# Kernel optimization log

Hardware: AMD Instinct MI355X
Metric: run time of the kernel (lower is better)

The kernel has to match this reference:

```python
import jax, jax.numpy as jnp
import numpy as np

GMAX, EMAX, NATOM, AA = 4, 10, 14, 20
SCALE_CLAMP = 0.1
EPS = 1e-8


def setup_inputs() -> dict:
    key = jax.random.key(0)
    ks = jax.random.split(key, 10)
    B, N, H = 4, 16384, 256
    rng = np.random.default_rng(0)
    # per-AA kinematic metadata (mimics pack_residue_meta_for_batch output)
    G_counts = rng.integers(1, GMAX + 1, size=AA).astype(np.int32)
    tors_axis = np.full((AA, GMAX, 2), -1, np.int32)
    aff_idx = np.zeros((AA, GMAX, EMAX), np.int32)
    aff_mask = np.zeros((AA, GMAX, EMAX), bool)
    for a in range(AA):
        for g in range(int(G_counts[a])):
            tors_axis[a, g] = rng.permutation(NATOM)[:2]
            perm = rng.permutation(NATOM)[:EMAX]  # unique affected atoms
            ne = int(rng.integers(3, EMAX + 1))
            aff_idx[a, g, :ne] = perm[:ne]
            aff_mask[a, g, :ne] = True
    scale_mask = rng.random((AA, NATOM)) < 0.5
    scale_parent = rng.integers(0, NATOM, size=(AA, NATOM)).astype(np.int32)

    s = 0.05
    ap = jax.random.uniform(ks[1], (B, N, AA), jnp.float32)
    return {
        'h': jax.random.normal(ks[0], (B, N, H), jnp.float32),
        'aatype_probs': ap / ap.sum(-1, keepdims=True),
        'X': jax.random.normal(ks[2], (B, N, NATOM, 3), jnp.float32),
        'W1': jax.random.normal(ks[3], (H + AA, H), jnp.float32) * s,
        'b1': jnp.zeros((H,), jnp.float32),
        'W2': jax.random.normal(ks[4], (H, H), jnp.float32) * s,
        'b2': jnp.zeros((H,), jnp.float32),
        'Wt': jax.random.normal(ks[5], (H, GMAX), jnp.float32) * s,
        'bt': jnp.zeros((GMAX,), jnp.float32),
        'Ws': jax.random.normal(ks[6], (H, NATOM), jnp.float32) * s,
        'bs': jnp.zeros((NATOM,), jnp.float32),
        'exists': jax.random.uniform(ks[7], (B, N, NATOM)) < 0.9,
        'top_idx': jax.random.randint(ks[8], (B, N), 0, AA, jnp.int32),
        'tors_axis': jnp.asarray(tors_axis),
        'aff_idx': jnp.asarray(aff_idx),
        'aff_mask': jnp.asarray(aff_mask),
        'G_counts': jnp.asarray(G_counts),
        'scale_mask': jnp.asarray(scale_mask),
        'scale_parent': jnp.asarray(scale_parent),
    }


def _take(X, idx):
    # X: [B,N,14,3], idx: [B,N,K] -> [B,N,K,3]
    return jnp.take_along_axis(X, jnp.broadcast_to(idx[..., None], idx.shape + (3,)), axis=2)


def _fk(X, exists, dchi, sraw, top_idx, TA, AI, AM, GC, SM, SP):
    B, N = top_idx.shape
    bi = jnp.arange(B)[:, None, None]
    ni = jnp.arange(N)[None, :, None]
    g_mask = jnp.arange(GMAX) < GC[..., None]  # [B,N,Gmax]
    for gi in range(GMAX):
        u, v = TA[..., gi, 0], TA[..., gi, 1]
        axis_ok = (u >= 0) & (v >= 0) & g_mask[..., gi]
        Pu = _take(X, jnp.maximum(u, 0)[..., None])  # [B,N,1,3]
        Pv = _take(X, jnp.maximum(v, 0)[..., None])
        axis = Pv - Pu
        axisn = axis / jnp.maximum(jnp.linalg.norm(axis, axis=-1, keepdims=True), EPS)
        ang = jnp.where(axis_ok, dchi[..., gi], 0.0)[..., None, None]  # [B,N,1,1]
        cols = jnp.maximum(AI[..., gi, :], 0)  # [B,N,E]
        cmask = AM[..., gi, :]
        Xa = _take(X, cols)          # [B,N,E,3]
        Va = Xa - Pu
        cos, sin = jnp.cos(ang), jnp.sin(ang)
        cross = jnp.cross(jnp.broadcast_to(axisn, Va.shape), Va, axis=-1)
        dot = jnp.sum(Va * axisn, -1, keepdims=True)
        Xa_new = Pu + Va * cos + cross * sin + axisn * dot * (1.0 - cos)
        ex_cols = jnp.take_along_axis(exists, cols, axis=2)
        wmask = cmask & ex_cols
        safe_cols = jnp.where(wmask, cols, NATOM)  # OOB -> dropped
        X = X.at[bi, ni, safe_cols].set(Xa_new, mode='drop')
    # bond-length scaling toward parent atom
    SPc = jnp.maximum(SP, 0)
    Pp = _take(X, SPc)               # [B,N,14,3]
    vvec = X - Pp
    r = jnp.maximum(jnp.linalg.norm(vvec, axis=-1, keepdims=True), EPS)
    dirv = vvec / r
    s_eff = jnp.clip(sraw, -1.0, 1.0) * SCALE_CLAMP
    Pa_new = Pp + dirv * r * (1.0 + s_eff[..., None])
    pair_exist = exists & jnp.take_along_axis(exists, SPc, axis=2)
    W = (SM & pair_exist)[..., None]
    return jnp.where(W, Pa_new, X)


def reference(h, aatype_probs, X, W1, b1, W2, b2, Wt, bt, Ws, bs,
              exists, top_idx, tors_axis, aff_idx, aff_mask, G_counts,
              scale_mask, scale_parent):
    # TorsionScaleHead
    z = jnp.concatenate([h, aatype_probs], axis=-1)
    z = jax.nn.silu(z @ W1 + b1)
    z = jax.nn.silu(z @ W2 + b2)
    dchi = jnp.tanh(z @ Wt + bt) * 0.5      # [B,N,Gmax]
    sraw = jnp.tanh(z @ Ws + bs)            # [B,N,14]
    # gather per-residue metadata
    TA = tors_axis[top_idx]
    AI = aff_idx[top_idx]
    AM = aff_mask[top_idx]
    GC = G_counts[top_idx]
    SM = scale_mask[top_idx]
    SP = scale_parent[top_idx]
    return _fk(X, exists, dchi, sraw, top_idx, TA, AI, AM, GC, SM, SP)
```

## Files before the change

kernel.cpp:

```cpp
#include <hip/hip_runtime.h>
#include <hip/hip_bf16.h>
#include <stdint.h>

#define TM 64
#define NT 512
#define HDIM 256
#define HA 276
#define HAP 288
#define ZROW 296
#define AAC 20
#define GMAXC 4
#define EMAXC 10
#define NATOMC 14

#define W1T_OFF 0
#define W2T_OFF 73728
#define W3T_OFF 139264
#define WS_ELEMS 147456

#define ZH_OFF  0
#define ZL_OFF  37888
#define XS_OFF  37888
#define EXS_OFF 48640
#define TSS_OFF 75776
#define SMEM_BYTES 80640

typedef __attribute__((ext_vector_type(8))) short bf16x8;
typedef __attribute__((ext_vector_type(4))) short short4v;
typedef __attribute__((ext_vector_type(4))) float f32x4;

__device__ __forceinline__ float silu_f(float x) {
    return x * (1.0f / (1.0f + __expf(-x)));
}

__device__ __forceinline__ float tanh_fast(float x) {
    float e = __expf(2.0f * x);
    return 1.0f - 2.0f / (e + 1.0f);
}

__device__ __forceinline__ unsigned short f2bf(float f) {
    union { float f; unsigned int u; } x; x.f = f;
    unsigned int r = x.u + 0x7fffu + ((x.u >> 16) & 1u);
    return (unsigned short)(r >> 16);
}

__device__ __forceinline__ float bf2f(unsigned short s) {
    union { unsigned int u; float f; } x; x.u = ((unsigned int)s) << 16;
    return x.f;
}

template <bool SPLIT>
__global__ __launch_bounds__(256) void prep_weights(
    const float* __restrict__ W1, const float* __restrict__ W2,
    const float* __restrict__ Wt, const float* __restrict__ Ws,
    unsigned short* __restrict__ ws)
{
    int idx = blockIdx.x * 256 + threadIdx.x;
    if (idx >= WS_ELEMS) return;
    float v;
    if (idx < W2T_OFF) {
        int n = idx / HAP, k = idx - n * HAP;
        v = (k < HA) ? W1[(size_t)k * HDIM + n] : 0.0f;
    } else if (idx < W3T_OFF) {
        int i = idx - W2T_OFF;
        int n = i / HDIM, k = i - n * HDIM;
        v = W2[(size_t)k * HDIM + n];
    } else {
        int i = idx - W3T_OFF;
        int n = i / HDIM, k = i - n * HDIM;
        v = (n < GMAXC) ? Wt[(size_t)k * GMAXC + n]
          : (n < GMAXC + NATOMC) ? Ws[(size_t)k * NATOMC + (n - GMAXC)]
          : 0.0f;
    }
    unsigned short hi = f2bf(v);
    ws[idx] = hi;
    if (SPLIT) ws[WS_ELEMS + idx] = f2bf(v - bf2f(hi));
}

template <bool SPLIT>
__global__ __launch_bounds__(NT, 4) void fused_refiner(
    const float* __restrict__ h,
    const float* __restrict__ probs,
    const float* __restrict__ X,
    const unsigned short* __restrict__ ws,
    const float* __restrict__ b1,
    const float* __restrict__ b2,
    const float* __restrict__ bt,
    const float* __restrict__ bs,
    const int* __restrict__ exists,
    const int* __restrict__ top_idx,
    const int* __restrict__ TA,
    const int* __restrict__ AI,
    const int* __restrict__ AM,
    const int* __restrict__ GC,
    const int* __restrict__ SM,
    const int* __restrict__ SP,
    float* __restrict__ out)
{
    __shared__ __align__(16) unsigned char smem[SMEM_BYTES];
    unsigned short (*zh)[ZROW] = (unsigned short (*)[ZROW])(smem + ZH_OFF);
    unsigned short (*zl)[ZROW] = (unsigned short (*)[ZROW])(smem + ZL_OFF);
    float (*tsS)[19]           = (float (*)[19])(smem + TSS_OFF);
    float (*Xs)[NATOMC][3]     = (float (*)[NATOMC][3])(smem + XS_OFF);
    uint8_t (*exS)[NATOMC]     = (uint8_t (*)[NATOMC])(smem + EXS_OFF);

    const int tid  = threadIdx.x;
    const int tok0 = blockIdx.x * TM;

    const int wv   = tid >> 6;
    const int ln   = tid & 63;
    const int ln16 = ln & 15;
    const int kg   = ln >> 4;
    const int nc0  = wv * 32;

    {
        const float4* h4 = reinterpret_cast<const float4*>(h + (size_t)tok0 * HDIM);
        for (int idx = tid; idx < TM * (HDIM / 4); idx += NT) {
            int t  = idx >> 6;
            int kq = idx & 63;
            float4 v = h4[(size_t)t * (HDIM / 4) + kq];
            short4v sh, sl;
            unsigned short a;
            a = f2bf(v.x); sh.x = (short)a; sl.x = (short)f2bf(v.x - bf2f(a));
            a = f2bf(v.y); sh.y = (short)a; sl.y = (short)f2bf(v.y - bf2f(a));
            a = f2bf(v.z); sh.z = (short)a; sl.z = (short)f2bf(v.z - bf2f(a));
            a = f2bf(v.w); sh.w = (short)a; sl.w = (short)f2bf(v.w - bf2f(a));
            *reinterpret_cast<short4v*>(&zh[t][kq * 4]) = sh;
            *reinterpret_cast<short4v*>(&zl[t][kq * 4]) = sl;
        }
        for (int idx = tid; idx < TM * AAC; idx += NT) {
            int t = idx / AAC;
            int p = idx - t * AAC;
            float v = probs[(size_t)(tok0 + t) * AAC + p];
            unsigned short a = f2bf(v);
            zh[t][HDIM + p] = a;
            zl[t][HDIM + p] = f2bf(v - bf2f(a));
        }
        for (int idx = tid; idx < TM * (ZROW - HA); idx += NT) {
            int t = idx / (ZROW - HA);
            int p = idx - t * (ZROW - HA);
            zh[t][HA + p] = 0;
            zl[t][HA + p] = 0;
        }
    }
    __syncthreads();

    const unsigned short* Wh = ws;
    const unsigned short* Wl = ws + WS_ELEMS;

    {
        f32x4 acc[4][2];
        #pragma unroll
        for (int m = 0; m < 4; ++m)
            #pragma unroll
            for (int n = 0; n < 2; ++n) acc[m][n] = (f32x4){0.f, 0.f, 0.f, 0.f};

        const size_t wbase = (size_t)(nc0 + ln16) * HAP + kg * 8 + W1T_OFF;
        #pragma unroll
        for (int kc = 0; kc < 9; ++kc) {
            const int kk = kc * 32 + kg * 8;
            bf16x8 ah[4], al[4];
            #pragma unroll
            for (int m = 0; m < 4; ++m) {
                ah[m] = *reinterpret_cast<const bf16x8*>(&zh[m * 16 + ln16][kk]);
                al[m] = *reinterpret_cast<const bf16x8*>(&zl[m * 16 + ln16][kk]);
            }
            #pragma unroll
            for (int n = 0; n < 2; ++n) {
                const size_t wo = wbase + kc * 32 + (size_t)n * 16 * HAP;
                bf16x8 bh = *reinterpret_cast<const bf16x8*>(Wh + wo);
                #pragma unroll
                for (int m = 0; m < 4; ++m)
                    acc[m][n] = __builtin_amdgcn_mfma_f32_16x16x32_bf16(ah[m], bh, acc[m][n], 0, 0, 0);
                #pragma unroll
                for (int m = 0; m < 4; ++m)
                    acc[m][n] = __builtin_amdgcn_mfma_f32_16x16x32_bf16(al[m], bh, acc[m][n], 0, 0, 0);
                if (SPLIT) {
                    bf16x8 bl = *reinterpret_cast<const bf16x8*>(Wl + wo);
                    #pragma unroll
                    for (int m = 0; m < 4; ++m)
                        acc[m][n] = __builtin_amdgcn_mfma_f32_16x16x32_bf16(ah[m], bl, acc[m][n], 0, 0, 0);
                }
            }
        }
        __syncthreads();
        #pragma unroll
        for (int n = 0; n < 2; ++n) {
            const int col = nc0 + n * 16 + ln16;
            const float bias = b1[col];
            #pragma unroll
            for (int m = 0; m < 4; ++m) {
                #pragma unroll
                for (int r = 0; r < 4; ++r) {
                    const int row = m * 16 + kg * 4 + r;
                    float val = silu_f(acc[m][n][r] + bias);
                    unsigned short hi = f2bf(val);
                    zh[row][col] = hi;
                    zl[row][col] = f2bf(val - bf2f(hi));
                }
            }
        }
    }
    __syncthreads();

    {
        f32x4 acc[4][2];
        #pragma unroll
        for (int m = 0; m < 4; ++m)
            #pragma unroll
            for (int n = 0; n < 2; ++n) acc[m][n] = (f32x4){0.f, 0.f, 0.f, 0.f};

        const size_t wbase = (size_t)(nc0 + ln16) * HDIM + kg * 8 + W2T_OFF;
        #pragma unroll
        for (int kc = 0; kc < 8; ++kc) {
            const int kk = kc * 32 + kg * 8;
            bf16x8 ah[4], al[4];
            #pragma unroll
            for (int m = 0; m < 4; ++m) {
                ah[m] = *reinterpret_cast<const bf16x8*>(&zh[m * 16 + ln16][kk]);
                al[m] = *reinterpret_cast<const bf16x8*>(&zl[m * 16 + ln16][kk]);
            }
            #pragma unroll
            for (int n = 0; n < 2; ++n) {
                const size_t wo = wbase + kc * 32 + (size_t)n * 16 * HDIM;
                bf16x8 bh = *reinterpret_cast<const bf16x8*>(Wh + wo);
                #pragma unroll
                for (int m = 0; m < 4; ++m)
                    acc[m][n] = __builtin_amdgcn_mfma_f32_16x16x32_bf16(ah[m], bh, acc[m][n], 0, 0, 0);
                #pragma unroll
                for (int m = 0; m < 4; ++m)
                    acc[m][n] = __builtin_amdgcn_mfma_f32_16x16x32_bf16(al[m], bh, acc[m][n], 0, 0, 0);
                if (SPLIT) {
                    bf16x8 bl = *reinterpret_cast<const bf16x8*>(Wl + wo);
                    #pragma unroll
                    for (int m = 0; m < 4; ++m)
                        acc[m][n] = __builtin_amdgcn_mfma_f32_16x16x32_bf16(ah[m], bl, acc[m][n], 0, 0, 0);
                }
            }
        }
        __syncthreads();
        #pragma unroll
        for (int n = 0; n < 2; ++n) {
            const int col = nc0 + n * 16 + ln16;
            const float bias = b2[col];
            #pragma unroll
            for (int m = 0; m < 4; ++m) {
                #pragma unroll
                for (int r = 0; r < 4; ++r) {
                    const int row = m * 16 + kg * 4 + r;
                    float val = silu_f(acc[m][n][r] + bias);
                    unsigned short hi = f2bf(val);
                    zh[row][col] = hi;
                    zl[row][col] = f2bf(val - bf2f(hi));
                }
            }
        }
    }
    __syncthreads();

    {
        const int m3 = wv & 3;
        const int n3 = wv >> 2;
        f32x4 acc = (f32x4){0.f, 0.f, 0.f, 0.f};
        const size_t wbase = (size_t)(n3 * 16 + ln16) * HDIM + kg * 8 + W3T_OFF;
        #pragma unroll
        for (int kc = 0; kc < 8; ++kc) {
            const int kk = kc * 32 + kg * 8;
            bf16x8 ah = *reinterpret_cast<const bf16x8*>(&zh[m3 * 16 + ln16][kk]);
            bf16x8 al = *reinterpret_cast<const bf16x8*>(&zl[m3 * 16 + ln16][kk]);
            const size_t wo = wbase + kc * 32;
            bf16x8 bh = *reinterpret_cast<const bf16x8*>(Wh + wo);
            acc = __builtin_amdgcn_mfma_f32_16x16x32_bf16(ah, bh, acc, 0, 0, 0);
            acc = __builtin_amdgcn_mfma_f32_16x16x32_bf16(al, bh, acc, 0, 0, 0);
            if (SPLIT) {
                bf16x8 bl = *reinterpret_cast<const bf16x8*>(Wl + wo);
                acc = __builtin_amdgcn_mfma_f32_16x16x32_bf16(ah, bl, acc, 0, 0, 0);
            }
        }
        const int o = n3 * 16 + ln16;
        if (o < GMAXC + NATOMC) {
            const float bias = (o < GMAXC) ? bt[o] : bs[o - GMAXC];
            #pragma unroll
            for (int r = 0; r < 4; ++r) {
                const int tok = m3 * 16 + kg * 4 + r;
                float val = tanh_fast(acc[r] + bias);
                if (o < GMAXC) val *= 0.5f;
                tsS[tok][o] = val;
            }
        }
    }
    __syncthreads();

    {
        float* Xsf = &Xs[0][0][0];
        for (int idx = tid; idx < TM * NATOMC * 3; idx += NT) {
            Xsf[idx] = X[(size_t)tok0 * NATOMC * 3 + idx];
        }
        uint8_t* exf = &exS[0][0];
        for (int idx = tid; idx < TM * NATOMC; idx += NT) {
            exf[idx] = (uint8_t)(exists[(size_t)tok0 * NATOMC + idx] != 0);
        }
    }
    __syncthreads();

    {
        const int t_loc = ln >> 3;
        const int r     = ln & 7;
        const int t     = wv * 8 + t_loc;
        const int a     = top_idx[tok0 + t];

        for (int gi = 0; gi < GMAXC; ++gi) {
            const int u  = TA[a * 8 + gi * 2 + 0];
            const int v  = TA[a * 8 + gi * 2 + 1];
            const int gc = GC[a];
            const bool axis_ok = (u >= 0) && (v >= 0) && (gi < gc);
            const int iu = u > 0 ? u : 0;
            const int iv = v > 0 ? v : 0;
            const float pux = Xs[t][iu][0], puy = Xs[t][iu][1], puz = Xs[t][iu][2];
            float ax = Xs[t][iv][0] - pux;
            float ay = Xs[t][iv][1] - puy;
            float az = Xs[t][iv][2] - puz;
            const float nrm = sqrtf(ax * ax + ay * ay + az * az);
            const float inv = 1.0f / fmaxf(nrm, 1e-8f);
            const float nx = ax * inv, ny = ay * inv, nz = az * inv;
            const float ang = axis_ok ? tsS[t][gi] : 0.0f;
            float sn, cs;
            __sincosf(ang, &sn, &cs);
            const float omc = 1.0f - cs;

            float newp[2][3];
            int   cidx[2];
            bool  wf[2];
            #pragma unroll
            for (int q = 0; q < 2; ++q) {
                const int e = r + q * 8;
                wf[q] = false; cidx[q] = 0;
                if (e < EMAXC) {
                    const int craw = AI[a * 40 + gi * 10 + e];
                    const int c = craw > 0 ? craw : 0;
                    const bool m = AM[a * 40 + gi * 10 + e] != 0;
                    const float vx = Xs[t][c][0] - pux;
                    const float vy = Xs[t][c][1] - puy;
                    const float vz = Xs[t][c][2] - puz;
                    const float dt  = vx * nx + vy * ny + vz * nz;
                    const float crx = ny * vz - nz * vy;
                    const float cry = nz * vx - nx * vz;
                    const float crz = nx * vy - ny * vx;
                    newp[q][0] = pux + vx * cs + crx * sn + nx * dt * omc;
                    newp[q][1] = puy + vy * cs + cry * sn + ny * dt * omc;
                    newp[q][2] = puz + vz * cs + crz * sn + nz * dt * omc;
                    const bool exc = exS[t][c] != 0;
                    wf[q] = m && exc;
                    cidx[q] = c;
                }
            }
            #pragma unroll
            for (int q = 0; q < 2; ++q) {
                if (wf[q]) {
                    Xs[t][cidx[q]][0] = newp[q][0];
                    Xs[t][cidx[q]][1] = newp[q][1];
                    Xs[t][cidx[q]][2] = newp[q][2];
                }
            }
        }

        #pragma unroll
        for (int q = 0; q < 2; ++q) {
            const int e = r + q * 8;
            if (e < NATOMC) {
                const int praw = SP[a * 14 + e];
                const int p = praw > 0 ? praw : 0;
                const float ppx = Xs[t][p][0], ppy = Xs[t][p][1], ppz = Xs[t][p][2];
                const float vx = Xs[t][e][0] - ppx;
                const float vy = Xs[t][e][1] - ppy;
                const float vz = Xs[t][e][2] - ppz;
                const float sr = tsS[t][GMAXC + e];
                const float se = fminf(fmaxf(sr, -1.f), 1.f) * 0.1f;
                const float f = 1.0f + se;
                const bool w = (SM[a * 14 + e] != 0) && (exS[t][e] != 0) && (exS[t][p] != 0);
                const float ox = w ? (ppx + vx * f) : Xs[t][e][0];
                const float oy = w ? (ppy + vy * f) : Xs[t][e][1];
                const float oz = w ? (ppz + vz * f) : Xs[t][e][2];
                const size_t ob = ((size_t)(tok0 + t) * NATOMC + e) * 3;
                out[ob + 0] = ox;
                out[ob + 1] = oy;
                out[ob + 2] = oz;
            }
        }
    }
}

extern "C" void kernel_launch(void* const* d_in, const int* in_sizes, int n_in,
                              void* d_out, int out_size, void* d_ws, size_t ws_size,
                              hipStream_t stream) {
    const float* h      = (const float*)d_in[0];
    const float* probs  = (const float*)d_in[1];
    const float* X      = (const float*)d_in[2];
    const float* W1     = (const float*)d_in[3];
    const float* b1     = (const float*)d_in[4];
    const float* W2     = (const float*)d_in[5];
    const float* b2     = (const float*)d_in[6];
    const float* Wt     = (const float*)d_in[7];
    const float* bt     = (const float*)d_in[8];
    const float* Ws     = (const float*)d_in[9];
    const float* bs     = (const float*)d_in[10];
    const int*   exists = (const int*)d_in[11];
    const int*   tidx   = (const int*)d_in[12];
    const int*   TA     = (const int*)d_in[13];
    const int*   AI     = (const int*)d_in[14];
    const int*   AM     = (const int*)d_in[15];
    const int*   GC     = (const int*)d_in[16];
    const int*   SM     = (const int*)d_in[17];
    const int*   SP     = (const int*)d_in[18];
    float*       out    = (float*)d_out;
    unsigned short* ws  = (unsigned short*)d_ws;

    const int BN = in_sizes[12];
    const int grid = BN / TM;
    const size_t need_split = (size_t)2 * WS_ELEMS * sizeof(unsigned short);

    if (ws_size >= need_split) {
        prep_weights<true><<<(WS_ELEMS + 255) / 256, 256, 0, stream>>>(W1, W2, Wt, Ws, ws);
        fused_refiner<true><<<grid, NT, 0, stream>>>(h, probs, X, ws, b1, b2, bt, bs,
                                                     exists, tidx, TA, AI, AM, GC, SM, SP, out);
    } else {
        prep_weights<false><<<(WS_ELEMS + 255) / 256, 256, 0, stream>>>(W1, W2, Wt, Ws, ws);
        fused_refiner<false><<<grid, NT, 0, stream>>>(h, probs, X, ws, b1, b2, bt, bs,
                                                      exists, tidx, TA, AI, AM, GC, SM, SP, out);
    }
}
```

Before: 109.7 us.

## Switch MLP GEMMs to 32x32x16 MFMA with weight prefetch and hw bf16 convert

Replaces the 16x16x32 bf16 MFMA tiling in all three GEMM stages with 32x32x16 MFMA tiles. Each wave now keeps two 32x32 accumulators, prefetches the next weight fragment one k-step ahead, and raises wave priority around the MFMA bursts. The hi/lo split conversion now uses the hardware bf16 conversion for the high part and truncation for the residual, which cuts ALU work but slightly changes rounding of the low term. The final head stage now runs on only two waves, each computing a 32-token by 32-output tile.

```diff
diff --git a/kernel.cpp b/kernel.cpp
--- a/kernel.cpp
+++ b/kernel.cpp
@@ -28,6 +28,7 @@
 typedef __attribute__((ext_vector_type(8))) short bf16x8;
 typedef __attribute__((ext_vector_type(4))) short short4v;
 typedef __attribute__((ext_vector_type(4))) float f32x4;
+typedef __attribute__((ext_vector_type(16))) float f32x16;
 
 __device__ __forceinline__ float silu_f(float x) {
     return x * (1.0f / (1.0f + __expf(-x)));
@@ -42,6 +43,17 @@
     union { float f; unsigned int u; } x; x.f = f;
     unsigned int r = x.u + 0x7fffu + ((x.u >> 16) & 1u);
     return (unsigned short)(r >> 16);
+}
+
+__device__ __forceinline__ unsigned short f2bf_hw(float f) {
+    union { __hip_bfloat16 b; unsigned short u; } x;
+    x.b = __float2bfloat16(f);
+    return x.u;
+}
+
+__device__ __forceinline__ unsigned short f2bf_trunc(float f) {
+    union { float f; unsigned int u; } x; x.f = f;
+    return (unsigned short)(x.u >> 16);
 }
 
 __device__ __forceinline__ float bf2f(unsigned short s) {
@@ -109,8 +121,8 @@
 
     const int wv   = tid >> 6;
     const int ln   = tid & 63;
-    const int ln16 = ln & 15;
-    const int kg   = ln >> 4;
+    const int ln31 = ln & 31;
+    const int kgb  = ln >> 5;
     const int nc0  = wv * 32;
 
     {
@@ -121,10 +133,10 @@
             float4 v = h4[(size_t)t * (HDIM / 4) + kq];
             short4v sh, sl;
             unsigned short a;
-            a = f2bf(v.x); sh.x = (short)a; sl.x = (short)f2bf(v.x - bf2f(a));
-            a = f2bf(v.y); sh.y = (short)a; sl.y = (short)f2bf(v.y - bf2f(a));
-            a = f2bf(v.z); sh.z = (short)a; sl.z = (short)f2bf(v.z - bf2f(a));
-            a = f2bf(v.w); sh.w = (short)a; sl.w = (short)f2bf(v.w - bf2f(a));
+            a = f2bf_hw(v.x); sh.x = (short)a; sl.x = (short)f2bf_trunc(v.x - bf2f(a));
+            a = f2bf_hw(v.y); sh.y = (short)a; sl.y = (short)f2bf_trunc(v.y - bf2f(a));
+            a = f2bf_hw(v.z); sh.z = (short)a; sl.z = (short)f2bf_trunc(v.z - bf2f(a));
+            a = f2bf_hw(v.w); sh.w = (short)a; sl.w = (short)f2bf_trunc(v.w - bf2f(a));
             *reinterpret_cast<short4v*>(&zh[t][kq * 4]) = sh;
             *reinterpret_cast<short4v*>(&zl[t][kq * 4]) = sl;
         }
@@ -132,9 +144,9 @@
             int t = idx / AAC;
             int p = idx - t * AAC;
             float v = probs[(size_t)(tok0 + t) * AAC + p];
-            unsigned short a = f2bf(v);
+            unsigned short a = f2bf_hw(v);
             zh[t][HDIM + p] = a;
-            zl[t][HDIM + p] = f2bf(v - bf2f(a));
+            zl[t][HDIM + p] = f2bf_trunc(v - bf2f(a));
         }
         for (int idx = tid; idx < TM * (ZROW - HA); idx += NT) {
             int t = idx / (ZROW - HA);
@@ -149,140 +161,138 @@
     const unsigned short* Wl = ws + WS_ELEMS;
 
     {
-        f32x4 acc[4][2];
-        #pragma unroll
-        for (int m = 0; m < 4; ++m)
-            #pragma unroll
-            for (int n = 0; n < 2; ++n) acc[m][n] = (f32x4){0.f, 0.f, 0.f, 0.f};
-
-        const size_t wbase = (size_t)(nc0 + ln16) * HAP + kg * 8 + W1T_OFF;
-        #pragma unroll
-        for (int kc = 0; kc < 9; ++kc) {
-            const int kk = kc * 32 + kg * 8;
-            bf16x8 ah[4], al[4];
-            #pragma unroll
-            for (int m = 0; m < 4; ++m) {
-                ah[m] = *reinterpret_cast<const bf16x8*>(&zh[m * 16 + ln16][kk]);
-                al[m] = *reinterpret_cast<const bf16x8*>(&zl[m * 16 + ln16][kk]);
-            }
-            #pragma unroll
-            for (int n = 0; n < 2; ++n) {
-                const size_t wo = wbase + kc * 32 + (size_t)n * 16 * HAP;
-                bf16x8 bh = *reinterpret_cast<const bf16x8*>(Wh + wo);
+        f32x16 acc[2];
+        #pragma unroll
+        for (int m = 0; m < 2; ++m)
+            #pragma unroll
+            for (int r = 0; r < 16; ++r) acc[m][r] = 0.f;
+
+        const size_t wbase = (size_t)(nc0 + ln31) * HAP + kgb * 8 + W1T_OFF;
+        bf16x8 nbh = *reinterpret_cast<const bf16x8*>(Wh + wbase);
+        bf16x8 nbl = {};
+        if (SPLIT) nbl = *reinterpret_cast<const bf16x8*>(Wl + wbase);
+        #pragma unroll
+        for (int kc = 0; kc < 18; ++kc) {
+            const bf16x8 bh = nbh, bl = nbl;
+            if (kc + 1 < 18) {
+                const size_t wn = wbase + (size_t)(kc + 1) * 16;
+                nbh = *reinterpret_cast<const bf16x8*>(Wh + wn);
+                if (SPLIT) nbl = *reinterpret_cast<const bf16x8*>(Wl + wn);
+            }
+            const int kk = kc * 16 + kgb * 8;
+            bf16x8 ah0 = *reinterpret_cast<const bf16x8*>(&zh[ln31][kk]);
+            bf16x8 ah1 = *reinterpret_cast<const bf16x8*>(&zh[32 + ln31][kk]);
+            bf16x8 al0 = *reinterpret_cast<const bf16x8*>(&zl[ln31][kk]);
+            bf16x8 al1 = *reinterpret_cast<const bf16x8*>(&zl[32 + ln31][kk]);
+            __builtin_amdgcn_s_setprio(1);
+            acc[0] = __builtin_amdgcn_mfma_f32_32x32x16_bf16(ah0, bh, acc[0], 0, 0, 0);
+            acc[1] = __builtin_amdgcn_mfma_f32_32x32x16_bf16(ah1, bh, acc[1], 0, 0, 0);
+            acc[0] = __builtin_amdgcn_mfma_f32_32x32x16_bf16(al0, bh, acc[0], 0, 0, 0);
+            acc[1] = __builtin_amdgcn_mfma_f32_32x32x16_bf16(al1, bh, acc[1], 0, 0, 0);
+            if (SPLIT) {
+                acc[0] = __builtin_amdgcn_mfma_f32_32x32x16_bf16(ah0, bl, acc[0], 0, 0, 0);
+                acc[1] = __builtin_amdgcn_mfma_f32_32x32x16_bf16(ah1, bl, acc[1], 0, 0, 0);
+            }
+            __builtin_amdgcn_s_setprio(0);
+        }
+        __syncthreads();
+        {
+            const int col = nc0 + ln31;
+            const float bias = b1[col];
+            #pragma unroll
+            for (int m = 0; m < 2; ++m) {
                 #pragma unroll
-                for (int m = 0; m < 4; ++m)
-                    acc[m][n] = __builtin_amdgcn_mfma_f32_16x16x32_bf16(ah[m], bh, acc[m][n], 0, 0, 0);
+                for (int r = 0; r < 16; ++r) {
+                    const int row = m * 32 + (r & 3) + 8 * (r >> 2) + 4 * kgb;
+                    float val = silu_f(acc[m][r] + bias);
+                    unsigned short hi = f2bf_hw(val);
+                    zh[row][col] = hi;
+                    zl[row][col] = f2bf_trunc(val - bf2f(hi));
+                }
+            }
+        }
+    }
+    __syncthreads();
+
+    {
+        f32x16 acc[2];
+        #pragma unroll
+        for (int m = 0; m < 2; ++m)
+            #pragma unroll
+            for (int r = 0; r < 16; ++r) acc[m][r] = 0.f;
+
+        const size_t wbase = (size_t)(nc0 + ln31) * HDIM + kgb * 8 + W2T_OFF;
+        bf16x8 nbh = *reinterpret_cast<const bf16x8*>(Wh + wbase);
+        bf16x8 nbl = {};
+        if (SPLIT) nbl = *reinterpret_cast<const bf16x8*>(Wl + wbase);
+        #pragma unroll
+        for (int kc = 0; kc < 16; ++kc) {
+            const bf16x8 bh = nbh, bl = nbl;
+            if (kc + 1 < 16) {
+                const size_t wn = wbase + (size_t)(kc + 1) * 16;
+                nbh = *reinterpret_cast<const bf16x8*>(Wh + wn);
+                if (SPLIT) nbl = *reinterpret_cast<const bf16x8*>(Wl + wn);
+            }
+            const int kk = kc * 16 + kgb * 8;
+            bf16x8 ah0 = *reinterpret_cast<const bf16x8*>(&zh[ln31][kk]);
+            bf16x8 ah1 = *reinterpret_cast<const bf16x8*>(&zh[32 + ln31][kk]);
+            bf16x8 al0 = *reinterpret_cast<const bf16x8*>(&zl[ln31][kk]);
+            bf16x8 al1 = *reinterpret_cast<const bf16x8*>(&zl[32 + ln31][kk]);
+            __builtin_amdgcn_s_setprio(1);
+            acc[0] = __builtin_amdgcn_mfma_f32_32x32x16_bf16(ah0, bh, acc[0], 0, 0, 0);
+            acc[1] = __builtin_amdgcn_mfma_f32_32x32x16_bf16(ah1, bh, acc[1], 0, 0, 0);
+            acc[0] = __builtin_amdgcn_mfma_f32_32x32x16_bf16(al0, bh, acc[0], 0, 0, 0);
+            acc[1] = __builtin_amdgcn_mfma_f32_32x32x16_bf16(al1, bh, acc[1], 0, 0, 0);
+            if (SPLIT) {
+                acc[0] = __builtin_amdgcn_mfma_f32_32x32x16_bf16(ah0, bl, acc[0], 0, 0, 0);
+                acc[1] = __builtin_amdgcn_mfma_f32_32x32x16_bf16(ah1, bl, acc[1], 0, 0, 0);
+            }
+            __builtin_amdgcn_s_setprio(0);
+        }
+        __syncthreads();
+        {
+            const int col = nc0 + ln31;
+            const float bias = b2[col];
+            #pragma unroll
+            for (int m = 0; m < 2; ++m) {
                 #pragma unroll
-                for (int m = 0; m < 4; ++m)
-                    acc[m][n] = __builtin_amdgcn_mfma_f32_16x16x32_bf16(al[m], bh, acc[m][n], 0, 0, 0);
-                if (SPLIT) {
-                    bf16x8 bl = *reinterpret_cast<const bf16x8*>(Wl + wo);
-                    #pragma unroll
-                    for (int m = 0; m < 4; ++m)
-                        acc[m][n] = __builtin_amdgcn_mfma_f32_16x16x32_bf16(ah[m], bl, acc[m][n], 0, 0, 0);
+                for (int r = 0; r < 16; ++r) {
+                    const int row = m * 32 + (r & 3) + 8 * (r >> 2) + 4 * kgb;
+                    float val = silu_f(acc[m][r] + bias);
+                    unsigned short hi = f2bf_hw(val);
+                    zh[row][col] = hi;
+                    zl[row][col] = f2bf_trunc(val - bf2f(hi));
                 }
             }
         }
-        __syncthreads();
-        #pragma unroll
-        for (int n = 0; n < 2; ++n) {
-            const int col = nc0 + n * 16 + ln16;
-            const float bias = b1[col];
-            #pragma unroll
-            for (int m = 0; m < 4; ++m) {
-                #pragma unroll
-                for (int r = 0; r < 4; ++r) {
-                    const int row = m * 16 + kg * 4 + r;
-                    float val = silu_f(acc[m][n][r] + bias);
-                    unsigned short hi = f2bf(val);
-                    zh[row][col] = hi;
-                    zl[row][col] = f2bf(val - bf2f(hi));
-                }
-            }
-        }
     }
     __syncthreads();
 
-    {
-        f32x4 acc[4][2];
-        #pragma unroll
-        for (int m = 0; m < 4; ++m)
-            #pragma unroll
-            for (int n = 0; n < 2; ++n) acc[m][n] = (f32x4){0.f, 0.f, 0.f, 0.f};
-
-        const size_t wbase = (size_t)(nc0 + ln16) * HDIM + kg * 8 + W2T_OFF;
-        #pragma unroll
-        for (int kc = 0; kc < 8; ++kc) {
-            const int kk = kc * 32 + kg * 8;
-            bf16x8 ah[4], al[4];
-            #pragma unroll
-            for (int m = 0; m < 4; ++m) {
-                ah[m] = *reinterpret_cast<const bf16x8*>(&zh[m * 16 + ln16][kk]);
-                al[m] = *reinterpret_cast<const bf16x8*>(&zl[m * 16 + ln16][kk]);
-            }
-            #pragma unroll
-            for (int n = 0; n < 2; ++n) {
-                const size_t wo = wbase + kc * 32 + (size_t)n * 16 * HDIM;
-                bf16x8 bh = *reinterpret_cast<const bf16x8*>(Wh + wo);
-                #pragma unroll
-                for (int m = 0; m < 4; ++m)
-                    acc[m][n] = __builtin_amdgcn_mfma_f32_16x16x32_bf16(ah[m], bh, acc[m][n], 0, 0, 0);
-                #pragma unroll
-                for (int m = 0; m < 4; ++m)
-                    acc[m][n] = __builtin_amdgcn_mfma_f32_16x16x32_bf16(al[m], bh, acc[m][n], 0, 0, 0);
-                if (SPLIT) {
-                    bf16x8 bl = *reinterpret_cast<const bf16x8*>(Wl + wo);
-                    #pragma unroll
-                    for (int m = 0; m < 4; ++m)
-                        acc[m][n] = __builtin_amdgcn_mfma_f32_16x16x32_bf16(ah[m], bl, acc[m][n], 0, 0, 0);
-                }
-            }
-        }
-        __syncthreads();
-        #pragma unroll
-        for (int n = 0; n < 2; ++n) {
-            const int col = nc0 + n * 16 + ln16;
-            const float bias = b2[col];
-            #pragma unroll
-            for (int m = 0; m < 4; ++m) {
-                #pragma unroll
-                for (int r = 0; r < 4; ++r) {
-                    const int row = m * 16 + kg * 4 + r;
-                    float val = silu_f(acc[m][n][r] + bias);
-                    unsigned short hi = f2bf(val);
-                    zh[row][col] = hi;
-                    zl[row][col] = f2bf(val - bf2f(hi));
-                }
-            }
-        }
-    }
-    __syncthreads();
-
-    {
-        const int m3 = wv & 3;
-        const int n3 = wv >> 2;
-        f32x4 acc = (f32x4){0.f, 0.f, 0.f, 0.f};
-        const size_t wbase = (size_t)(n3 * 16 + ln16) * HDIM + kg * 8 + W3T_OFF;
-        #pragma unroll
-        for (int kc = 0; kc < 8; ++kc) {
-            const int kk = kc * 32 + kg * 8;
-            bf16x8 ah = *reinterpret_cast<const bf16x8*>(&zh[m3 * 16 + ln16][kk]);
-            bf16x8 al = *reinterpret_cast<const bf16x8*>(&zl[m3 * 16 + ln16][kk]);
-            const size_t wo = wbase + kc * 32;
+    if (wv < 2) {
+        f32x16 acc;
+        #pragma unroll
+        for (int r = 0; r < 16; ++r) acc[r] = 0.f;
+        const size_t wbase = (size_t)ln31 * HDIM + kgb * 8 + W3T_OFF;
+        #pragma unroll
+        for (int kc = 0; kc < 16; ++kc) {
+            const int kk = kc * 16 + kgb * 8;
+            bf16x8 ah = *reinterpret_cast<const bf16x8*>(&zh[wv * 32 + ln31][kk]);
+            bf16x8 al = *reinterpret_cast<const bf16x8*>(&zl[wv * 32 + ln31][kk]);
+            const size_t wo = wbase + (size_t)kc * 16;
             bf16x8 bh = *reinterpret_cast<const bf16x8*>(Wh + wo);
-            acc = __builtin_amdgcn_mfma_f32_16x16x32_bf16(ah, bh, acc, 0, 0, 0);
-            acc = __builtin_amdgcn_mfma_f32_16x16x32_bf16(al, bh, acc, 0, 0, 0);
+            acc = __builtin_amdgcn_mfma_f32_32x32x16_bf16(ah, bh, acc, 0, 0, 0);
+            acc = __builtin_amdgcn_mfma_f32_32x32x16_bf16(al, bh, acc, 0, 0, 0);
             if (SPLIT) {
                 bf16x8 bl = *reinterpret_cast<const bf16x8*>(Wl + wo);
-                acc = __builtin_amdgcn_mfma_f32_16x16x32_bf16(ah, bl, acc, 0, 0, 0);
-            }
-        }
-        const int o = n3 * 16 + ln16;
+                acc = __builtin_amdgcn_mfma_f32_32x32x16_bf16(ah, bl, acc, 0, 0, 0);
+            }
+        }
+        const int o = ln31;
         if (o < GMAXC + NATOMC) {
             const float bias = (o < GMAXC) ? bt[o] : bs[o - GMAXC];
             #pragma unroll
-            for (int r = 0; r < 4; ++r) {
-                const int tok = m3 * 16 + kg * 4 + r;
+            for (int r = 0; r < 16; ++r) {
+                const int tok = wv * 32 + (r & 3) + 8 * (r >> 2) + 4 * kgb;
                 float val = tanh_fast(acc[r] + bias);
                 if (o < GMAXC) val *= 0.5f;
                 tsS[tok][o] = val;
```

Result: slower. 116.0 us (+5.7%).
